# Optimization experiments

Measured on AMD Instinct MI355X. Metric: run time of the kernel, lower is better.

## Reference

```python
import jax, jax.numpy as jnp
import numpy as np

N = 10000   # nodes
K = 8       # out-degree per node (uniform)
E = N * K   # edges
D = 64      # d_embed (also per-head dim: projection is d_embed -> d_embed*n_heads)
H = 8       # n_heads
DE = 16     # d_e_embed (also per-edge-head dim)
EH = 4      # e_heads
EPS = 1e-16


def seg_softmax(src, index, num):
    # torch_geometric.utils.softmax: per-segment max-subtract, exp, normalize
    mx = jax.ops.segment_max(src, index, num_segments=num)
    mx = jnp.where(jnp.isfinite(mx), mx, 0.0)
    ex = jnp.exp(src - mx[index])
    s = jax.ops.segment_sum(ex, index, num_segments=num)
    return ex / (s[index] + EPS)


def _lin(k, out_d, in_d):
    # xavier-uniform-ish weight, zero bias (matches init_weights)
    bound = float(np.sqrt(6.0 / (in_d + out_d)))
    W = jax.random.uniform(k, (out_d, in_d), jnp.float32, -bound, bound)
    return W, jnp.zeros((out_d,), jnp.float32)


def setup_inputs() -> dict:
    key = jax.random.key(0)
    ks = jax.random.split(key, 12)
    x = jax.random.normal(ks[0], (N, D), jnp.float32)
    row0 = jnp.repeat(jnp.arange(N, dtype=jnp.int32), K)          # sorted sources
    row1 = jax.random.randint(ks[1], (E,), 0, N, jnp.int32)        # random targets
    edge_index = jnp.stack([row0, row1])                           # [2, E]
    # n^3 pair indices (uniform degree => closed form matching torch helper)
    eiq = jnp.repeat(jnp.arange(E, dtype=jnp.int32), K)            # repeat_interleave within node block
    eik = jnp.broadcast_to(jnp.arange(E, dtype=jnp.int32).reshape(N, 1, K), (N, K, K)).reshape(-1)  # tile within block
    edge_features = jax.random.normal(ks[2], (E, DE), jnp.float32)
    Wq, bq = _lin(ks[3], D * H, D)
    Wk, bk = _lin(ks[4], D * H, D)
    Wv, bv = _lin(ks[5], D * H, D)
    Wlin, blin = _lin(ks[6], D, H * D)
    Weq, beq = _lin(ks[7], DE * EH, DE)
    Wev, bev = _lin(ks[8], DE * EH, DE)
    Wek, bek = _lin(ks[9], DE * EH, H)
    Wel, bel = _lin(ks[10], H, EH * DE)
    Wele, bele = _lin(ks[11], DE, H)
    return dict(x=x, edge_features=edge_features,
                Wq=Wq, bq=bq, Wk=Wk, bk=bk, Wv=Wv, bv=bv, Wlin=Wlin, blin=blin,
                Weq=Weq, beq=beq, Wev=Wev, bev=bev, Wek=Wek, bek=bek,
                Wel=Wel, bel=bel, Wele=Wele, bele=bele,
                edge_index=edge_index, eiq=eiq, eik=eik)


def reference(x, edge_features, Wq, bq, Wk, bk, Wv, bv, Wlin, blin,
              Weq, beq, Wev, bev, Wek, bek, Wel, bel, Wele, bele,
              edge_index, eiq, eik):
    e0, e1 = edge_index[0], edge_index[1]
    nq = (x @ Wq.T + bq).reshape(N, H, D)
    nk = (x @ Wk.T + bk).reshape(N, H, D)
    nv = (x @ Wv.T + bv).reshape(N, H, D)
    # per-edge scaled dot product: [E, H]
    sqk = (nq[e0] * nk[e1]).sum(-1) / jnp.sqrt(jnp.float32(D))
    # --- edge attention over edge-edge pairs ---
    eq = (edge_features @ Weq.T + beq).reshape(E, EH, DE)
    ev = (edge_features @ Wev.T + bev).reshape(E, EH, DE)
    ek = (sqk @ Wek.T + bek).reshape(E, EH, DE)
    seqk = (eq[eiq] * ek[eik]).sum(-1) / jnp.sqrt(jnp.float32(DE))   # [P, EH]
    att_e = seg_softmax(seqk, eiq, E)
    eout = jax.ops.segment_sum(att_e[:, :, None] * ev[eik], eiq, num_segments=E)  # [E, EH, DE]
    edge_emb = eout.reshape(E, EH * DE) @ Wel.T + bel                # [E, H]
    # --- node attention with edge-modulated scores ---
    att_n = seg_softmax(edge_emb + sqk, e0, N)                       # [E, H]
    node = jax.ops.segment_sum(att_n[:, :, None] * nv[e1], e0, num_segments=N)    # [N, H, D]
    node_embeddings = node.reshape(N, H * D) @ Wlin.T + blin         # [N, D]
    edge_embeddings = edge_emb @ Wele.T + bele                       # [E, DE]
    return node_embeddings, edge_embeddings
```

## Files before the change

kernel.cpp:

```cpp
#include <hip/hip_runtime.h>

typedef unsigned short u16;
typedef unsigned int   u32;

#define N_NODES 10000
#define N_EDGES 80000

typedef __attribute__((ext_vector_type(8))) short bf16x8;
typedef __attribute__((ext_vector_type(4))) float fx4;
#define MFMA16(a, b, c) __builtin_amdgcn_mfma_f32_16x16x32_bf16(a, b, c, 0, 0, 0)

__device__ __forceinline__ u16 f2bf(float f) {
    union { float f; u32 i; } c; c.f = f;
    u32 u = c.i;
    u32 r = (u + 0x7fffu + ((u >> 16) & 1u)) >> 16;
    return (u16)r;
}
__device__ __forceinline__ float bf2f(u16 u) {
    union { u32 i; float f; } c; c.i = ((u32)u) << 16; return c.f;
}
__device__ __forceinline__ void unpack8(uint4 w, float* v) {
    union { u32 i; float f; } c;
    c.i = w.x << 16; v[0] = c.f; c.i = w.x & 0xffff0000u; v[1] = c.f;
    c.i = w.y << 16; v[2] = c.f; c.i = w.y & 0xffff0000u; v[3] = c.f;
    c.i = w.z << 16; v[4] = c.f; c.i = w.z & 0xffff0000u; v[5] = c.f;
    c.i = w.w << 16; v[6] = c.f; c.i = w.w & 0xffff0000u; v[7] = c.f;
}


__device__ __forceinline__ void stage_w(const float* src, int rstride,
                                        u16* wh, u16* wl, int t) {
    const int row = t >> 2, seg = t & 3;
    const float* p = src + (long)row * rstride + seg * 16;
    float v[16];
    #pragma unroll
    for (int q = 0; q < 4; ++q) *(float4*)&v[q * 4] = *(const float4*)(p + q * 4);
    u16 hh[16], ll[16];
    #pragma unroll
    for (int j = 0; j < 16; ++j) {
        u16 hi = f2bf(v[j]);
        hh[j] = hi;
        ll[j] = f2bf(v[j] - bf2f(hi));
    }
    const int base = row * 72 + seg * 16;
    *(uint4*)&wh[base]     = *(uint4*)&hh[0];
    *(uint4*)&wh[base + 8] = *(uint4*)&hh[8];
    *(uint4*)&wl[base]     = *(uint4*)&ll[0];
    *(uint4*)&wl[base + 8] = *(uint4*)&ll[8];
}

__device__ __forceinline__ void load_a64(const float* m, int arow, int ko,
                                         bf16x8 ah[2], bf16x8 al[2]) {
    if (arow < N_NODES) {
        #pragma unroll
        for (int ks = 0; ks < 2; ++ks) {
            const float* p = m + (long)arow * 64 + ks * 32 + ko;
            float v[8];
            *(float4*)&v[0] = *(const float4*)p;
            *(float4*)&v[4] = *(const float4*)(p + 4);
            #pragma unroll
            for (int j = 0; j < 8; ++j) {
                u16 hi = f2bf(v[j]);
                ah[ks][j] = (short)hi;
                al[ks][j] = (short)f2bf(v[j] - bf2f(hi));
            }
        }
    } else {
        #pragma unroll
        for (int ks = 0; ks < 2; ++ks) { ah[ks] = (bf16x8)0; al[ks] = (bf16x8)0; }
    }
}

__device__ __forceinline__ fx4 gemm3(const bf16x8 ah[2], const bf16x8 al[2],
                                     const u16* wh, const u16* wl,
                                     int colrow, int ko) {
    fx4 acc = {0.f, 0.f, 0.f, 0.f};
    #pragma unroll
    for (int ks = 0; ks < 2; ++ks) {
        const bf16x8 bh = *(const bf16x8*)&wh[colrow * 72 + ks * 32 + ko];
        const bf16x8 bl = *(const bf16x8*)&wl[colrow * 72 + ks * 32 + ko];
        acc = MFMA16(al[ks], bh, acc);
        acc = MFMA16(ah[ks], bl, acc);
        acc = MFMA16(ah[ks], bh, acc);
    }
    return acc;
}

__global__ __launch_bounds__(256) void projkvg_kernel(
    const float* __restrict__ x,
    const float* __restrict__ Wk, const float* __restrict__ bk,
    const float* __restrict__ Wv, const float* __restrict__ bv,
    const float* __restrict__ Wlin,
    u16* __restrict__ NK, u16* __restrict__ G)
{
    __shared__ __align__(16) u16 wh[64 * 72];
    __shared__ __align__(16) u16 wl[64 * 72];
    __shared__ __align__(16) u16 nvh[4 * 16 * 72];
    __shared__ __align__(16) u16 nvl[4 * 16 * 72];

    const int t  = threadIdx.x;
    const int l  = t & 63, w = t >> 6;
    const int ko = (l >> 4) * 8;
    const int r0 = blockIdx.x * 64;
    const int cy = blockIdx.y;
    const bool kq = (cy < 8);
    const int c0 = (kq ? cy : (cy - 8)) * 64;

    bf16x8 ah[2], al[2];
    load_a64(x, r0 + w * 16 + (l & 15), ko, ah, al);

    stage_w(kq ? (Wk + (long)c0 * 64) : (Wv + (long)c0 * 64), 64, wh, wl, t);
    __syncthreads();

    fx4 acc[4];
    #pragma unroll
    for (int cf = 0; cf < 4; ++cf)
        acc[cf] = gemm3(ah, al, wh, wl, cf * 16 + (l & 15), ko);

    if (kq) {
        #pragma unroll
        for (int cf = 0; cf < 4; ++cf) {
            const int col = c0 + cf * 16 + (l & 15);
            const float bias = bk[col];
            #pragma unroll
            for (int j = 0; j < 4; ++j) {
                const int gr = r0 + w * 16 + (l >> 4) * 4 + j;
                if (gr < N_NODES) NK[(long)gr * 512 + col] = f2bf(acc[cf][j] + bias);
            }
        }
        return;
    }

    #pragma unroll
    for (int cf = 0; cf < 4; ++cf) {
        const int col = cf * 16 + (l & 15);
        const float bias = bv[c0 + col];
        #pragma unroll
        for (int j = 0; j < 4; ++j) {
            const int rloc = (l >> 4) * 4 + j;
            float v = acc[cf][j] + bias;
            u16 hi = f2bf(v);
            nvh[w * 1152 + rloc * 72 + col] = hi;
            nvl[w * 1152 + rloc * 72 + col] = f2bf(v - bf2f(hi));
        }
    }
    __syncthreads();
    stage_w(Wlin + c0, 512, wh, wl, t);
    __syncthreads();

    bf16x8 a2h[2], a2l[2];
    #pragma unroll
    for (int ks = 0; ks < 2; ++ks) {
        a2h[ks] = *(const bf16x8*)&nvh[w * 1152 + (l & 15) * 72 + ks * 32 + ko];
        a2l[ks] = *(const bf16x8*)&nvl[w * 1152 + (l & 15) * 72 + ks * 32 + ko];
    }
    #pragma unroll
    for (int cf = 0; cf < 4; ++cf)
        acc[cf] = gemm3(a2h, a2l, wh, wl, cf * 16 + (l & 15), ko);

    #pragma unroll
    for (int cf = 0; cf < 4; ++cf) {
        const int col = c0 + cf * 16 + (l & 15);
        #pragma unroll
        for (int j = 0; j < 4; ++j) {
            const int gr = r0 + w * 16 + (l >> 4) * 4 + j;
            if (gr < N_NODES) G[(long)gr * 512 + col] = f2bf(acc[cf][j]);
        }
    }
}

__global__ __launch_bounds__(256) void sqk_kernel(
    const float* __restrict__ x, const float* __restrict__ Wq, const float* __restrict__ bq,
    const u16* __restrict__ NK, const int* __restrict__ e1, float* __restrict__ sq)
{
    __shared__ __align__(16) u16 wh[64 * 72];
    __shared__ __align__(16) u16 wl[64 * 72];
    __shared__ __align__(16) float qh[64 * 68];
    __shared__ int tg[512];

    const int t  = threadIdx.x;
    const int l  = t & 63, w = t >> 6;
    const int ko = (l >> 4) * 8;
    const int n0 = blockIdx.x * 64;
    const int h  = blockIdx.y;

    bf16x8 ah[2], al[2];
    load_a64(x, n0 + w * 16 + (l & 15), ko, ah, al);
    stage_w(Wq + (long)h * 64 * 64, 64, wh, wl, t);
    {
        int i0 = t, i1 = t + 256;
        tg[i0] = (n0 * 8 + i0 < N_EDGES) ? e1[n0 * 8 + i0] : 0;
        tg[i1] = (n0 * 8 + i1 < N_EDGES) ? e1[n0 * 8 + i1] : 0;
    }
    __syncthreads();

    fx4 acc[4];
    #pragma unroll
    for (int cf = 0; cf < 4; ++cf)
        acc[cf] = gemm3(ah, al, wh, wl, cf * 16 + (l & 15), ko);

    #pragma unroll
    for (int cf = 0; cf < 4; ++cf) {
        const int col = cf * 16 + (l & 15);
        const float bias = bq[h * 64 + col];
        #pragma unroll
        for (int j = 0; j < 4; ++j)
            qh[(w * 16 + (l >> 4) * 4 + j) * 68 + col] = acc[cf][j] + bias;
    }
    __syncthreads();

    #pragma unroll
    for (int rep = 0; rep < 2; ++rep) {
        const int p = rep * 256 + t;
        const int nl = p >> 3, i = p & 7;
        if (n0 + nl < N_NODES) {
            const int kr = tg[p];
            const uint4* kp = (const uint4*)(NK + ((long)kr * 512 + h * 64));
            float d = 0.f;
            #pragma unroll
            for (int q4 = 0; q4 < 8; ++q4) {
                float kv[8]; unpack8(kp[q4], kv);
                float4 qa = *(const float4*)&qh[nl * 68 + q4 * 8];
                float4 qb = *(const float4*)&qh[nl * 68 + q4 * 8 + 4];
                d += qa.x * kv[0] + qa.y * kv[1] + qa.z * kv[2] + qa.w * kv[3]
                   + qb.x * kv[4] + qb.y * kv[5] + qb.z * kv[6] + qb.w * kv[7];
            }
            sq[(long)(n0 + nl) * 64 + i * 8 + h] = d * 0.125f;
        }
    }
}

__global__ __launch_bounds__(64) void node_kernel(
    const float* __restrict__ ef, const int* __restrict__ e1,
    const float* __restrict__ sq, const u16* __restrict__ G,
    const float* __restrict__ Weq, const float* __restrict__ beq,
    const float* __restrict__ Wev, const float* __restrict__ bev,
    const float* __restrict__ Wek, const float* __restrict__ bek,
    const float* __restrict__ Wel, const float* __restrict__ bel,
    const float* __restrict__ Wele, const float* __restrict__ bele,
    const float* __restrict__ blin,
    float* __restrict__ out_node, float* __restrict__ out_edge)
{
    __shared__ __align__(16) float sqk_l[64];
    __shared__ __align__(16) float efl[128];
    __shared__ __align__(16) float ebuf[4 * 8 * 68];
    __shared__ __align__(16) float sl[4 * 72];
    __shared__ __align__(16) float well[8 * 68];
    __shared__ __align__(16) float emb_l[64];
    __shared__ __align__(16) float attn_l[64];

    const int t = threadIdx.x;
    const int n = blockIdx.x;

    int tg[8];
    #pragma unroll
    for (int i = 0; i < 8; ++i) tg[i] = e1[n * 8 + i];

    sqk_l[t] = sq[(long)n * 64 + t];
    {
        const float2* p = (const float2*)(ef + (long)n * 128);
        float2 wv = p[t];
        efl[2 * t] = wv.x; efl[2 * t + 1] = wv.y;
    }
    for (int idx = t; idx < 512; idx += 64)
        well[(idx >> 6) * 68 + (idx & 63)] = Wel[idx];
    __syncthreads();

    float wq16[16], wv16[16], wk8[8];
    {
        const float4* p = (const float4*)(Weq + t * 16);
        #pragma unroll
        for (int q4 = 0; q4 < 4; ++q4) *(float4*)&wq16[q4 * 4] = p[q4];
        const float4* q = (const float4*)(Wev + t * 16);
        #pragma unroll
        for (int q4 = 0; q4 < 4; ++q4) *(float4*)&wv16[q4 * 4] = q[q4];
        const float4* r = (const float4*)(Wek + t * 8);
        *(float4*)&wk8[0] = r[0]; *(float4*)&wk8[4] = r[1];
    }
    const float beqv = beq[t], bevv = bev[t], bekv = bek[t];

    float* eqb = &ebuf[0];
    float* ekb = &ebuf[544];
    float* evb = &ebuf[1088];
    float* eob = &ebuf[1632];

    #pragma unroll
    for (int i = 0; i < 8; ++i) {
        float aq = beqv, av = bevv;
        #pragma unroll
        for (int q = 0; q < 4; ++q) {
            float4 f = *(const float4*)&efl[i * 16 + q * 4];
            aq += f.x * wq16[q * 4] + f.y * wq16[q * 4 + 1] + f.z * wq16[q * 4 + 2] + f.w * wq16[q * 4 + 3];
            av += f.x * wv16[q * 4] + f.y * wv16[q * 4 + 1] + f.z * wv16[q * 4 + 2] + f.w * wv16[q * 4 + 3];
        }
        float ak = bekv;
        #pragma unroll
        for (int q = 0; q < 2; ++q) {
            float4 s = *(const float4*)&sqk_l[i * 8 + q * 4];
            ak += s.x * wk8[q * 4] + s.y * wk8[q * 4 + 1] + s.z * wk8[q * 4 + 2] + s.w * wk8[q * 4 + 3];
        }
        eqb[i * 68 + t] = aq; evb[i * 68 + t] = av; ekb[i * 68 + t] = ak;
    }
    __syncthreads();

    {
        const int i = t >> 3, j = t & 7;
        #pragma unroll
        for (int eh = 0; eh < 4; ++eh) {
            float acc = 0.f;
            #pragma unroll
            for (int q = 0; q < 4; ++q) {
                float4 a = *(const float4*)&eqb[i * 68 + eh * 16 + q * 4];
                float4 b = *(const float4*)&ekb[j * 68 + eh * 16 + q * 4];
                acc += a.x * b.x + a.y * b.y + a.z * b.z + a.w * b.w;
            }
            sl[eh * 72 + i * 8 + j] = acc * 0.25f;
        }
    }
    __syncthreads();

    if (t < 32) {
        const int i = t >> 2, eh = t & 3;
        float4 v0 = *(const float4*)&sl[eh * 72 + i * 8];
        float4 v1 = *(const float4*)&sl[eh * 72 + i * 8 + 4];
        float mx = fmaxf(fmaxf(fmaxf(v0.x, v0.y), fmaxf(v0.z, v0.w)),
                         fmaxf(fmaxf(v1.x, v1.y), fmaxf(v1.z, v1.w)));
        float e0 = __expf(v0.x - mx), e1_ = __expf(v0.y - mx);
        float e2 = __expf(v0.z - mx), e3  = __expf(v0.w - mx);
        float e4 = __expf(v1.x - mx), e5  = __expf(v1.y - mx);
        float e6 = __expf(v1.z - mx), e7  = __expf(v1.w - mx);
        float inv = 1.f / (e0 + e1_ + e2 + e3 + e4 + e5 + e6 + e7 + 1e-16f);
        float4 w0 = {e0 * inv, e1_ * inv, e2 * inv, e3 * inv};
        float4 w1 = {e4 * inv, e5 * inv, e6 * inv, e7 * inv};
        *(float4*)&sl[eh * 72 + i * 8]     = w0;
        *(float4*)&sl[eh * 72 + i * 8 + 4] = w1;
    }
    __syncthreads();

    {
        const int eh = t >> 4;
        #pragma unroll
        for (int i = 0; i < 8; ++i) {
            float4 s0 = *(const float4*)&sl[eh * 72 + i * 8];
            float4 s1 = *(const float4*)&sl[eh * 72 + i * 8 + 4];
            float acc = s0.x * evb[0 * 68 + t] + s0.y * evb[1 * 68 + t]
                      + s0.z * evb[2 * 68 + t] + s0.w * evb[3 * 68 + t]
                      + s1.x * evb[4 * 68 + t] + s1.y * evb[5 * 68 + t]
                      + s1.z * evb[6 * 68 + t] + s1.w * evb[7 * 68 + t];
            eob[i * 68 + t] = acc;
        }
    }
    __syncthreads();

    {
        const int i = t >> 3, h = t & 7;
        float acc = bel[h];
        #pragma unroll
        for (int q = 0; q < 16; ++q) {
            float4 a  = *(const float4*)&eob[i * 68 + q * 4];
            float4 wv = *(const float4*)&well[h * 68 + q * 4];
            acc += a.x * wv.x + a.y * wv.y + a.z * wv.z + a.w * wv.w;
        }
        emb_l[i * 8 + h] = acc;
    }
    __syncthreads();

    uint4 greg[8];
    {
        const int i = t >> 3, c8 = t & 7;
        const uint4* gp = (const uint4*)(G + (long)tg[i] * 512);
        #pragma unroll
        for (int q = 0; q < 8; ++q) greg[q] = gp[c8 + q * 8];
    }

    #pragma unroll
    for (int rep = 0; rep < 2; ++rep) {
        const int idx = rep * 64 + t;
        const int i = idx >> 4, de = idx & 15;
        float acc = bele[de];
        #pragma unroll
        for (int h = 0; h < 8; ++h) acc += emb_l[i * 8 + h] * Wele[de * 8 + h];
        out_edge[(long)n * 128 + idx] = acc;
    }

    if (t < 8) {
        const int h = t;
        float lg[8], mx = -1e30f;
        #pragma unroll
        for (int i = 0; i < 8; ++i) { lg[i] = emb_l[i * 8 + h] + sqk_l[i * 8 + h]; mx = fmaxf(mx, lg[i]); }
        float sum = 0.f;
        #pragma unroll
        for (int i = 0; i < 8; ++i) { float e = __expf(lg[i] - mx); attn_l[i * 8 + h] = e; sum += e; }
        float inv = 1.f / (sum + 1e-16f);
        #pragma unroll
        for (int i = 0; i < 8; ++i) attn_l[i * 8 + h] *= inv;
    }

    u16* gbuf = (u16*)ebuf;
    {
        const int i = t >> 3, c8 = t & 7;
        #pragma unroll
        for (int q = 0; q < 8; ++q)
            *(uint4*)&gbuf[i * 520 + (c8 + q * 8) * 8] = greg[q];
    }
    __syncthreads();

    {
        float acc = blin[t];
        #pragma unroll
        for (int i = 0; i < 8; ++i) {
            float4 a0 = *(const float4*)&attn_l[i * 8];
            float4 a1 = *(const float4*)&attn_l[i * 8 + 4];
            const u16* gr = &gbuf[i * 520];
            acc += a0.x * bf2f(gr[0 * 64 + t]) + a0.y * bf2f(gr[1 * 64 + t])
                 + a0.z * bf2f(gr[2 * 64 + t]) + a0.w * bf2f(gr[3 * 64 + t])
                 + a1.x * bf2f(gr[4 * 64 + t]) + a1.y * bf2f(gr[5 * 64 + t])
                 + a1.z * bf2f(gr[6 * 64 + t]) + a1.w * bf2f(gr[7 * 64 + t]);
        }
        out_node[(long)n * 64 + t] = acc;
    }
}

extern "C" void kernel_launch(void* const* d_in, const int* in_sizes, int n_in,
                              void* d_out, int out_size, void* d_ws, size_t ws_size,
                              hipStream_t stream) {
    (void)in_sizes; (void)n_in; (void)out_size; (void)ws_size;
    const float* x    = (const float*)d_in[0];
    const float* ef   = (const float*)d_in[1];
    const float* Wq   = (const float*)d_in[2];
    const float* bq   = (const float*)d_in[3];
    const float* Wk   = (const float*)d_in[4];
    const float* bk   = (const float*)d_in[5];
    const float* Wv   = (const float*)d_in[6];
    const float* bv   = (const float*)d_in[7];
    const float* Wlin = (const float*)d_in[8];
    const float* blin = (const float*)d_in[9];
    const float* Weq  = (const float*)d_in[10];
    const float* beq  = (const float*)d_in[11];
    const float* Wev  = (const float*)d_in[12];
    const float* bev  = (const float*)d_in[13];
    const float* Wek  = (const float*)d_in[14];
    const float* bek  = (const float*)d_in[15];
    const float* Wel  = (const float*)d_in[16];
    const float* bel  = (const float*)d_in[17];
    const float* Wele = (const float*)d_in[18];
    const float* bele = (const float*)d_in[19];
    const int* edge_index = (const int*)d_in[20];
    const int* e1 = edge_index + N_EDGES;

    float* out_node = (float*)d_out;
    float* out_edge = (float*)d_out + 640000;

    char* ws = (char*)d_ws;
    u16*   NK = (u16*)ws;
    u16*   G  = (u16*)(ws + 10240000);
    float* sq = (float*)(ws + 20480000);

    projkvg_kernel<<<dim3(157, 16), 256, 0, stream>>>(x, Wk, bk, Wv, bv, Wlin, NK, G);
    sqk_kernel<<<dim3(157, 8), 256, 0, stream>>>(x, Wq, bq, NK, e1, sq);
    node_kernel<<<N_NODES, 64, 0, stream>>>(ef, e1, sq, G,
                                            Weq, beq, Wev, bev, Wek, bek,
                                            Wel, bel, Wele, bele, blin,
                                            out_node, out_edge);
}
```

Baseline: 180.7 us.

## Fuse Q projection into proj kernel and compute edge scores in node kernel

The separate sqk kernel is removed. The projection kernel now computes Q, K and V for one head per block in sequence, writing Q as fp32 to workspace. The per-edge q·k scores are computed inside node_kernel, which reads the node's Q row and gathers K rows. This drops one launch and a recomputation pass, but writes and reads a full fp32 NQ tensor (about 20 MB) and halves the projection grid while doing more work per block.

```diff
diff --git a/kernel.cpp b/kernel.cpp
--- a/kernel.cpp
+++ b/kernel.cpp
@@ -86,12 +86,13 @@
     return acc;
 }
 
-__global__ __launch_bounds__(256) void projkvg_kernel(
+__global__ __launch_bounds__(256) void proj_kernel(
     const float* __restrict__ x,
+    const float* __restrict__ Wq, const float* __restrict__ bq,
     const float* __restrict__ Wk, const float* __restrict__ bk,
     const float* __restrict__ Wv, const float* __restrict__ bv,
     const float* __restrict__ Wlin,
-    u16* __restrict__ NK, u16* __restrict__ G)
+    float* __restrict__ NQ, u16* __restrict__ NK, u16* __restrict__ G)
 {
     __shared__ __align__(16) u16 wh[64 * 72];
     __shared__ __align__(16) u16 wl[64 * 72];
@@ -102,35 +103,53 @@
     const int l  = t & 63, w = t >> 6;
     const int ko = (l >> 4) * 8;
     const int r0 = blockIdx.x * 64;
-    const int cy = blockIdx.y;
-    const bool kq = (cy < 8);
-    const int c0 = (kq ? cy : (cy - 8)) * 64;
+    const int h  = blockIdx.y;
+    const int c0 = h * 64;
 
     bf16x8 ah[2], al[2];
     load_a64(x, r0 + w * 16 + (l & 15), ko, ah, al);
 
-    stage_w(kq ? (Wk + (long)c0 * 64) : (Wv + (long)c0 * 64), 64, wh, wl, t);
-    __syncthreads();
-
     fx4 acc[4];
+
+    stage_w(Wq + (long)c0 * 64, 64, wh, wl, t);
+    __syncthreads();
     #pragma unroll
     for (int cf = 0; cf < 4; ++cf)
         acc[cf] = gemm3(ah, al, wh, wl, cf * 16 + (l & 15), ko);
-
-    if (kq) {
-        #pragma unroll
-        for (int cf = 0; cf < 4; ++cf) {
-            const int col = c0 + cf * 16 + (l & 15);
-            const float bias = bk[col];
-            #pragma unroll
-            for (int j = 0; j < 4; ++j) {
-                const int gr = r0 + w * 16 + (l >> 4) * 4 + j;
-                if (gr < N_NODES) NK[(long)gr * 512 + col] = f2bf(acc[cf][j] + bias);
-            }
-        }
-        return;
-    }
-
+    #pragma unroll
+    for (int cf = 0; cf < 4; ++cf) {
+        const int col = c0 + cf * 16 + (l & 15);
+        const float bias = bq[col];
+        #pragma unroll
+        for (int j = 0; j < 4; ++j) {
+            const int gr = r0 + w * 16 + (l >> 4) * 4 + j;
+            if (gr < N_NODES) NQ[(long)gr * 512 + col] = acc[cf][j] + bias;
+        }
+    }
+    __syncthreads();
+
+    stage_w(Wk + (long)c0 * 64, 64, wh, wl, t);
+    __syncthreads();
+    #pragma unroll
+    for (int cf = 0; cf < 4; ++cf)
+        acc[cf] = gemm3(ah, al, wh, wl, cf * 16 + (l & 15), ko);
+    #pragma unroll
+    for (int cf = 0; cf < 4; ++cf) {
+        const int col = c0 + cf * 16 + (l & 15);
+        const float bias = bk[col];
+        #pragma unroll
+        for (int j = 0; j < 4; ++j) {
+            const int gr = r0 + w * 16 + (l >> 4) * 4 + j;
+            if (gr < N_NODES) NK[(long)gr * 512 + col] = f2bf(acc[cf][j] + bias);
+        }
+    }
+    __syncthreads();
+
+    stage_w(Wv + (long)c0 * 64, 64, wh, wl, t);
+    __syncthreads();
+    #pragma unroll
+    for (int cf = 0; cf < 4; ++cf)
+        acc[cf] = gemm3(ah, al, wh, wl, cf * 16 + (l & 15), ko);
     #pragma unroll
     for (int cf = 0; cf < 4; ++cf) {
         const int col = cf * 16 + (l & 15);
@@ -169,70 +188,10 @@
     }
 }
 
-__global__ __launch_bounds__(256) void sqk_kernel(
-    const float* __restrict__ x, const float* __restrict__ Wq, const float* __restrict__ bq,
-    const u16* __restrict__ NK, const int* __restrict__ e1, float* __restrict__ sq)
-{
-    __shared__ __align__(16) u16 wh[64 * 72];
-    __shared__ __align__(16) u16 wl[64 * 72];
-    __shared__ __align__(16) float qh[64 * 68];
-    __shared__ int tg[512];
-
-    const int t  = threadIdx.x;
-    const int l  = t & 63, w = t >> 6;
-    const int ko = (l >> 4) * 8;
-    const int n0 = blockIdx.x * 64;
-    const int h  = blockIdx.y;
-
-    bf16x8 ah[2], al[2];
-    load_a64(x, n0 + w * 16 + (l & 15), ko, ah, al);
-    stage_w(Wq + (long)h * 64 * 64, 64, wh, wl, t);
-    {
-        int i0 = t, i1 = t + 256;
-        tg[i0] = (n0 * 8 + i0 < N_EDGES) ? e1[n0 * 8 + i0] : 0;
-        tg[i1] = (n0 * 8 + i1 < N_EDGES) ? e1[n0 * 8 + i1] : 0;
-    }
-    __syncthreads();
-
-    fx4 acc[4];
-    #pragma unroll
-    for (int cf = 0; cf < 4; ++cf)
-        acc[cf] = gemm3(ah, al, wh, wl, cf * 16 + (l & 15), ko);
-
-    #pragma unroll
-    for (int cf = 0; cf < 4; ++cf) {
-        const int col = cf * 16 + (l & 15);
-        const float bias = bq[h * 64 + col];
-        #pragma unroll
-        for (int j = 0; j < 4; ++j)
-            qh[(w * 16 + (l >> 4) * 4 + j) * 68 + col] = acc[cf][j] + bias;
-    }
-    __syncthreads();
-
-    #pragma unroll
-    for (int rep = 0; rep < 2; ++rep) {
-        const int p = rep * 256 + t;
-        const int nl = p >> 3, i = p & 7;
-        if (n0 + nl < N_NODES) {
-            const int kr = tg[p];
-            const uint4* kp = (const uint4*)(NK + ((long)kr * 512 + h * 64));
-            float d = 0.f;
-            #pragma unroll
-            for (int q4 = 0; q4 < 8; ++q4) {
-                float kv[8]; unpack8(kp[q4], kv);
-                float4 qa = *(const float4*)&qh[nl * 68 + q4 * 8];
-                float4 qb = *(const float4*)&qh[nl * 68 + q4 * 8 + 4];
-                d += qa.x * kv[0] + qa.y * kv[1] + qa.z * kv[2] + qa.w * kv[3]
-                   + qb.x * kv[4] + qb.y * kv[5] + qb.z * kv[6] + qb.w * kv[7];
-            }
-            sq[(long)(n0 + nl) * 64 + i * 8 + h] = d * 0.125f;
-        }
-    }
-}
-
 __global__ __launch_bounds__(64) void node_kernel(
     const float* __restrict__ ef, const int* __restrict__ e1,
-    const float* __restrict__ sq, const u16* __restrict__ G,
+    const float* __restrict__ NQ, const u16* __restrict__ NK,
+    const u16* __restrict__ G,
     const float* __restrict__ Weq, const float* __restrict__ beq,
     const float* __restrict__ Wev, const float* __restrict__ bev,
     const float* __restrict__ Wek, const float* __restrict__ bek,
@@ -243,6 +202,7 @@
 {
     __shared__ __align__(16) float sqk_l[64];
     __shared__ __align__(16) float efl[128];
+    __shared__ __align__(16) float qrow[8 * 68];
     __shared__ __align__(16) float ebuf[4 * 8 * 68];
     __shared__ __align__(16) float sl[4 * 72];
     __shared__ __align__(16) float well[8 * 68];
@@ -256,7 +216,25 @@
     #pragma unroll
     for (int i = 0; i < 8; ++i) tg[i] = e1[n * 8 + i];
 
-    sqk_l[t] = sq[(long)n * 64 + t];
+    float wq16[16], wv16[16], wk8[8];
+    {
+        const float4* p = (const float4*)(Weq + t * 16);
+        #pragma unroll
+        for (int q4 = 0; q4 < 4; ++q4) *(float4*)&wq16[q4 * 4] = p[q4];
+        const float4* q = (const float4*)(Wev + t * 16);
+        #pragma unroll
+        for (int q4 = 0; q4 < 4; ++q4) *(float4*)&wv16[q4 * 4] = q[q4];
+        const float4* r = (const float4*)(Wek + t * 8);
+        *(float4*)&wk8[0] = r[0]; *(float4*)&wk8[4] = r[1];
+    }
+    const float beqv = beq[t], bevv = bev[t], bekv = bek[t];
+
+    {
+        const float4* p = (const float4*)(NQ + (long)n * 512);
+        const int h = t >> 3, d0 = (t & 7) * 8;
+        *(float4*)&qrow[h * 68 + d0]     = p[2 * t];
+        *(float4*)&qrow[h * 68 + d0 + 4] = p[2 * t + 1];
+    }
     {
         const float2* p = (const float2*)(ef + (long)n * 128);
         float2 wv = p[t];
@@ -266,18 +244,22 @@
         well[(idx >> 6) * 68 + (idx & 63)] = Wel[idx];
     __syncthreads();
 
-    float wq16[16], wv16[16], wk8[8];
-    {
-        const float4* p = (const float4*)(Weq + t * 16);
-        #pragma unroll
-        for (int q4 = 0; q4 < 4; ++q4) *(float4*)&wq16[q4 * 4] = p[q4];
-        const float4* q = (const float4*)(Wev + t * 16);
-        #pragma unroll
-        for (int q4 = 0; q4 < 4; ++q4) *(float4*)&wv16[q4 * 4] = q[q4];
-        const float4* r = (const float4*)(Wek + t * 8);
-        *(float4*)&wk8[0] = r[0]; *(float4*)&wk8[4] = r[1];
-    }
-    const float beqv = beq[t], bevv = bev[t], bekv = bek[t];
+    {
+        const int i = t >> 3, h = t & 7;
+        const uint4* kp = (const uint4*)(NK + ((long)tg[i] * 512 + h * 64));
+        const float* qp = &qrow[h * 68];
+        float d = 0.f;
+        #pragma unroll
+        for (int q4 = 0; q4 < 8; ++q4) {
+            float kv[8]; unpack8(kp[q4], kv);
+            float4 qa = *(const float4*)&qp[q4 * 8];
+            float4 qb = *(const float4*)&qp[q4 * 8 + 4];
+            d += qa.x * kv[0] + qa.y * kv[1] + qa.z * kv[2] + qa.w * kv[3]
+               + qb.x * kv[4] + qb.y * kv[5] + qb.z * kv[6] + qb.w * kv[7];
+        }
+        sqk_l[t] = d * 0.125f;
+    }
+    __syncthreads();
 
     float* eqb = &ebuf[0];
     float* ekb = &ebuf[544];
@@ -454,11 +436,11 @@
     char* ws = (char*)d_ws;
     u16*   NK = (u16*)ws;
     u16*   G  = (u16*)(ws + 10240000);
-    float* sq = (float*)(ws + 20480000);
-
-    projkvg_kernel<<<dim3(157, 16), 256, 0, stream>>>(x, Wk, bk, Wv, bv, Wlin, NK, G);
-    sqk_kernel<<<dim3(157, 8), 256, 0, stream>>>(x, Wq, bq, NK, e1, sq);
-    node_kernel<<<N_NODES, 64, 0, stream>>>(ef, e1, sq, G,
+    float* NQ = (float*)(ws + 20480000);
+
+    proj_kernel<<<dim3(157, 8), 256, 0, stream>>>(x, Wq, bq, Wk, bk, Wv, bv, Wlin,
+                                                  NQ, NK, G);
+    node_kernel<<<N_NODES, 64, 0, stream>>>(ef, e1, NQ, NK, G,
                                             Weq, beq, Wev, bev, Wek, bek,
                                             Wel, bel, Wele, bele, blin,
                                             out_node, out_edge);
```

After: 178.1 us. Within noise of the previous version (-1.5%).
